# Optimization experiments

Measured on AMD Instinct MI355X. Metric: run time of the kernel, lower is better.

The kernel has to match this reference:

```python
import jax, jax.numpy as jnp
import numpy as np

B, S, D = 1, 2048, 2048
HQ, HKV, DH = 16, 4, 128
WINDOW = 512  # sliding window encoded in explicit attn_mask


def rotate_half(u):
    u1, u2 = jnp.split(u, 2, axis=-1)
    return jnp.concatenate([-u2, u1], axis=-1)


def setup_inputs() -> dict:
    key = jax.random.key(0)
    ks = jax.random.split(key, 6)
    x = jax.random.normal(ks[0], (B, S, D), dtype=jnp.float32)
    # RoPE caches (standard rotary frequencies, full d_head with duplicated halves)
    pos = jnp.arange(S)
    inv_freq = 1.0 / (10000.0 ** (jnp.arange(0, DH, 2, dtype=jnp.float32) / DH))
    ang = pos[:, None].astype(jnp.float32) * inv_freq[None, :]  # [S, DH/2]
    emb = jnp.concatenate([ang, ang], axis=-1)                  # [S, DH]
    cos_cache = jnp.cos(emb)
    sin_cache = jnp.sin(emb)
    # sliding-window causal mask: attend to j<=i and i-j < WINDOW
    i = jnp.arange(S)[:, None]
    j = jnp.arange(S)[None, :]
    attn_mask = (j <= i) & ((i - j) < WINDOW)
    sc = 0.02
    Wq = jax.random.normal(ks[1], (D, HQ * DH), dtype=jnp.float32) * sc
    Wk = jax.random.normal(ks[2], (D, HKV * DH), dtype=jnp.float32) * sc
    Wv = jax.random.normal(ks[3], (D, HKV * DH), dtype=jnp.float32) * sc
    Wo = jax.random.normal(ks[4], (HQ * DH, D), dtype=jnp.float32) * sc
    return {"x": x, "cos_cache": cos_cache, "sin_cache": sin_cache,
            "positions": pos.astype(jnp.int64), "attn_mask": attn_mask,
            "Wq": Wq, "Wk": Wk, "Wv": Wv, "Wo": Wo}


def reference(x, cos_cache, sin_cache, positions, attn_mask, Wq, Wk, Wv, Wo):
    batch, seq_len, _ = x.shape
    Q = (x @ Wq).reshape(batch, seq_len, HQ, DH).transpose(0, 2, 1, 3)   # [B,HQ,S,DH]
    K = (x @ Wk).reshape(batch, seq_len, HKV, DH).transpose(0, 2, 1, 3)  # [B,HKV,S,DH]
    V = (x @ Wv).reshape(batch, seq_len, HKV, DH).transpose(0, 2, 1, 3)
    # RoPE
    cos = cos_cache[positions][None, None, :, :]  # [1,1,S,DH]
    sin = sin_cache[positions][None, None, :, :]
    Q = Q * cos + rotate_half(Q) * sin
    K = K * cos + rotate_half(K) * sin
    # GQA expansion (repeat_interleave along head dim)
    G = HQ // HKV
    K_exp = jnp.repeat(K, G, axis=1)  # [B,HQ,S,DH]
    V_exp = jnp.repeat(V, G, axis=1)
    scores = jnp.einsum('bhqd,bhkd->bhqk', Q, K_exp) / jnp.sqrt(jnp.float32(DH))
    neg_inf = jnp.finfo(scores.dtype).min
    scores = jnp.where(attn_mask[None, None, :, :], scores, neg_inf)
    weights = jax.nn.softmax(scores, axis=-1)
    attn_out = jnp.einsum('bhqk,bhkd->bhqd', weights, V_exp)
    attn_out = attn_out.transpose(0, 2, 1, 3).reshape(batch, seq_len, HQ * DH)
    output = attn_out @ Wo
    return (output, K, V)  # new kv cache is the (post-RoPE) K, V
```

## Files before the change

### kernel.cpp

```cpp
#include <hip/hip_runtime.h>
#include <stdint.h>

typedef unsigned short u16;
typedef __attribute__((ext_vector_type(4))) float f32x4;
typedef __attribute__((ext_vector_type(8))) short short8;
typedef __attribute__((ext_vector_type(4))) short short4v;

__device__ inline u16 f2bf(float f) {
  union { float f; uint32_t u; } v; v.f = f;
  uint32_t u = v.u;
  u += 0x7fffu + ((u >> 16) & 1u);
  return (u16)(u >> 16);
}
__device__ inline float bf2f(u16 b) {
  union { uint32_t u; float f; } v; v.u = (uint32_t)b << 16; return v.f;
}

__global__ __launch_bounds__(256) void k_prep(const float* __restrict__ x,
                                              const float* __restrict__ Wq, const float* __restrict__ Wk,
                                              const float* __restrict__ Wv, const float* __restrict__ Wo,
                                              u16* __restrict__ xb, u16* __restrict__ WT, u16* __restrict__ WoT) {
  const int b = blockIdx.x, tid = threadIdx.x;
  if (b < 1024) {
    size_t base = (size_t)b * 4096 + tid * 4;
    #pragma unroll
    for (int k = 0; k < 4; ++k) {
      f32x4 v = *(const f32x4*)(x + base + k * 1024);
      short4v o;
      o.x = (short)f2bf(v.x); o.y = (short)f2bf(v.y);
      o.z = (short)f2bf(v.z); o.w = (short)f2bf(v.w);
      *(short4v*)(xb + base + k * 1024) = o;
    }
    return;
  }
  __shared__ float t[64][68];
  const float* W; u16* D; int N, bb;
  if (b < 2048)      { W = Wq; D = WT;                       N = 2048; bb = b - 1024; }
  else if (b < 2304) { W = Wk; D = WT + (size_t)2048 * 2048; N = 512;  bb = b - 2048; }
  else if (b < 2560) { W = Wv; D = WT + (size_t)2560 * 2048; N = 512;  bb = b - 2304; }
  else               { W = Wo; D = WoT;                      N = 2048; bb = b - 2560; }
  const int nb = N >> 6;
  const int n0 = (bb % nb) * 64, k0 = (bb / nb) * 64;
  const int c4 = (tid & 15) * 4, rbase = tid >> 4;
  #pragma unroll
  for (int p = 0; p < 4; ++p) {
    int r = p * 16 + rbase;
    *(f32x4*)&t[r][c4] = *(const f32x4*)&W[(size_t)(k0 + r) * N + n0 + c4];
  }
  __syncthreads();
  const int i = tid >> 2, j = (tid & 3) * 16;
  short8 o0, o1;
  #pragma unroll
  for (int m = 0; m < 8; ++m) o0[m] = (short)f2bf(t[j + m][i]);
  #pragma unroll
  for (int m = 0; m < 8; ++m) o1[m] = (short)f2bf(t[j + 8 + m][i]);
  *(short8*)&D[(size_t)(n0 + i) * 2048 + k0 + j] = o0;
  *(short8*)&D[(size_t)(n0 + i) * 2048 + k0 + j + 8] = o1;
}

__global__ __launch_bounds__(512, 2) void k_gemmqkv(const u16* __restrict__ A,
                                                    const u16* __restrict__ B,
                                                    u16* __restrict__ C) {
  const int K = 2048;
  const int NT = 32;
  __shared__ __align__(16) u16 lds[3 * 20480];
  const int tid = threadIdx.x;
  const int wid = tid >> 6, lane = tid & 63;
  const int quad = lane >> 4, l16 = lane & 15;
  const int wm = (wid >> 2) * 64;
  const int wn = (wid & 3) * 48;
  const int bm = blockIdx.y * 128, bn = blockIdx.x * 192;

  const u16* aSrc[2]; int aDst[2];
  #pragma unroll
  for (int L = 0; L < 2; ++L) {
    int E = (tid + L * 512) * 8;
    int r = E >> 6, pc = (E >> 3) & 7;
    int lc = pc ^ (r & 7);
    aSrc[L] = A + (size_t)(bm + r) * K + lc * 8;
    aDst[L] = E;
  }
  const u16* bSrc[3]; int bDst[3];
  #pragma unroll
  for (int L = 0; L < 3; ++L) {
    int E = (tid + L * 512) * 8;
    int r = E >> 6, pc = (E >> 3) & 7;
    int lc = pc ^ (r & 7);
    bSrc[L] = B + (size_t)(bn + r) * K + lc * 8;
    bDst[L] = 8192 + E;
  }

  #define STAGE(buf, kt) do {                                                              \
    _Pragma("unroll")                                                                      \
    for (int L = 0; L < 2; ++L)                                                            \
      __builtin_amdgcn_global_load_lds(                                                    \
          (const __attribute__((address_space(1))) void*)(aSrc[L] + (kt) * 64),            \
          (__attribute__((address_space(3))) void*)(&lds[(buf) * 20480 + aDst[L]]), 16, 0, 0); \
    _Pragma("unroll")                                                                      \
    for (int L = 0; L < 3; ++L)                                                            \
      __builtin_amdgcn_global_load_lds(                                                    \
          (const __attribute__((address_space(1))) void*)(bSrc[L] + (kt) * 64),            \
          (__attribute__((address_space(3))) void*)(&lds[(buf) * 20480 + bDst[L]]), 16, 0, 0); \
  } while (0)

  f32x4 acc[4][3];
  #pragma unroll
  for (int m = 0; m < 4; ++m)
    #pragma unroll
    for (int n = 0; n < 3; ++n) acc[m][n] = (f32x4){0.f, 0.f, 0.f, 0.f};

  STAGE(0, 0);
  STAGE(1, 1);
  asm volatile("s_waitcnt vmcnt(5)" ::: "memory");
  __builtin_amdgcn_s_barrier();

  int c = 0, p = 2;
  for (int t = 0; t < NT; ++t) {
    if (t + 2 < NT) STAGE(p, t + 2);

    short8 af[4][2], bf[3][2];
    #pragma unroll
    for (int mf = 0; mf < 4; ++mf)
      #pragma unroll
      for (int kc = 0; kc < 2; ++kc) {
        int R = wm + mf * 16 + l16;
        int pc = (kc * 4 + quad) ^ (R & 7);
        af[mf][kc] = *(const short8*)&lds[c * 20480 + R * 64 + pc * 8];
      }
    #pragma unroll
    for (int nf = 0; nf < 3; ++nf)
      #pragma unroll
      for (int kc = 0; kc < 2; ++kc) {
        int Cc = wn + nf * 16 + l16;
        int pc = (kc * 4 + quad) ^ (Cc & 7);
        bf[nf][kc] = *(const short8*)&lds[c * 20480 + 8192 + Cc * 64 + pc * 8];
      }

    __builtin_amdgcn_s_setprio(1);
    #pragma unroll
    for (int mf = 0; mf < 4; ++mf)
      #pragma unroll
      for (int nf = 0; nf < 3; ++nf)
        #pragma unroll
        for (int kc = 0; kc < 2; ++kc)
          acc[mf][nf] = __builtin_amdgcn_mfma_f32_16x16x32_bf16(af[mf][kc], bf[nf][kc], acc[mf][nf], 0, 0, 0);
    __builtin_amdgcn_s_setprio(0);

    if (t + 2 < NT) {
      asm volatile("s_waitcnt vmcnt(5)" ::: "memory");
    } else if (t + 1 < NT) {
      asm volatile("s_waitcnt vmcnt(0)" ::: "memory");
    }
    __builtin_amdgcn_s_barrier();
    c = (c == 2) ? 0 : c + 1;
    p = (p == 2) ? 0 : p + 1;
  }
  #undef STAGE

  #pragma unroll
  for (int mf = 0; mf < 4; ++mf) {
    int row = bm + wm + mf * 16 + quad * 4;
    #pragma unroll
    for (int nf = 0; nf < 3; ++nf) {
      int col = bn + wn + nf * 16 + l16;
      #pragma unroll
      for (int r = 0; r < 4; ++r)
        C[(size_t)(row + r) * 3072 + col] = f2bf(acc[mf][nf][r]);
    }
  }
}

__global__ __launch_bounds__(256) void k_gemm64(const u16* __restrict__ A,
                                                const u16* __restrict__ B,
                                                u16* __restrict__ C,
                                                int M, int N, int K) {
  __shared__ u16 As[2][128 * 32];
  __shared__ u16 Bs[2][128 * 32];
  const int tid = threadIdx.x;
  const int wid = tid >> 6, lane = tid & 63;
  const int quad = lane >> 4, l16 = lane & 15;
  const int wm = (wid >> 1) * 64, wn = (wid & 1) * 64;
  const int bm = blockIdx.y * 128, bn = blockIdx.x * 128;
  const int lr = lane >> 2;
  const int lc = (lane & 3) * 8;
  const int kper = K / gridDim.z;
  const int kbeg = blockIdx.z * kper;
  u16* Cz = C + (size_t)blockIdx.z * M * N;

  f32x4 acc[4][4];
  #pragma unroll
  for (int mi = 0; mi < 4; ++mi)
    #pragma unroll
    for (int ni = 0; ni < 4; ++ni)
      acc[mi][ni] = (f32x4){0.f, 0.f, 0.f, 0.f};

  for (int k0 = kbeg; k0 < kbeg + kper; k0 += 64) {
    const u16* Ag = A + (size_t)bm * K + k0;
    const u16* Bg = B + (size_t)bn * K + k0;
    #pragma unroll
    for (int h = 0; h < 2; ++h)
      #pragma unroll
      for (int p = 0; p < 2; ++p) {
        const int r0 = wid * 32 + p * 16;
        const int rr = r0 + lr;
        __builtin_amdgcn_global_load_lds(
            (const __attribute__((address_space(1))) void*)(Ag + (size_t)rr * K + h * 32 + lc),
            (__attribute__((address_space(3))) void*)(&As[h][r0 * 32]),
            16, 0, 0);
        __builtin_amdgcn_global_load_lds(
            (const __attribute__((address_space(1))) void*)(Bg + (size_t)rr * K + h * 32 + lc),
            (__attribute__((address_space(3))) void*)(&Bs[h][r0 * 32]),
            16, 0, 0);
      }
    __syncthreads();
    #pragma unroll
    for (int h = 0; h < 2; ++h) {
      short8 af[4], bfr[4];
      #pragma unroll
      for (int i = 0; i < 4; ++i) {
        af[i]  = *(const short8*)&As[h][(wm + i * 16 + l16) * 32 + quad * 8];
        bfr[i] = *(const short8*)&Bs[h][(wn + i * 16 + l16) * 32 + quad * 8];
      }
      #pragma unroll
      for (int mi = 0; mi < 4; ++mi)
        #pragma unroll
        for (int ni = 0; ni < 4; ++ni)
          acc[mi][ni] = __builtin_amdgcn_mfma_f32_16x16x32_bf16(af[mi], bfr[ni], acc[mi][ni], 0, 0, 0);
    }
    __syncthreads();
  }
  #pragma unroll
  for (int mi = 0; mi < 4; ++mi) {
    int row = bm + wm + mi * 16 + quad * 4;
    #pragma unroll
    for (int ni = 0; ni < 4; ++ni) {
      int col = bn + wn + ni * 16 + l16;
      #pragma unroll
      for (int r = 0; r < 4; ++r)
        Cz[(size_t)(row + r) * N + col] = f2bf(acc[mi][ni][r]);
    }
  }
}

__global__ __launch_bounds__(256) void k_post(const u16* __restrict__ P,
                                              const float* __restrict__ cosc, const float* __restrict__ sinc,
                                              u16* __restrict__ Qb, u16* __restrict__ Kb, u16* __restrict__ Vt,
                                              float* __restrict__ Kout, float* __restrict__ Vout) {
  const int b = blockIdx.x, tid = threadIdx.x;
  if (b < 2048) {
    __shared__ float row[3072];
    const int s = b;
    const u16* p0 = P + (size_t)s * 3072;
    for (int i = tid * 4; i < 3072; i += 1024) {
      short4v a0 = *(const short4v*)(p0 + i);
      #pragma unroll
      for (int m = 0; m < 4; ++m)
        row[i + m] = bf2f((u16)a0[m]);
    }
    __syncthreads();
    const int d = tid & 127;
    const int hbase = tid >> 7;
    const float c = cosc[s * 128 + d], sn = sinc[s * 128 + d];
    const float scale = 0.08838834764831845f;
    #pragma unroll
    for (int it = 0; it < 12; ++it) {
      int slice = it * 2 + hbase;
      float v = row[slice * 128 + d];
      if (slice < 20) {
        float other = (d < 64) ? -row[slice * 128 + d + 64] : row[slice * 128 + d - 64];
        float r = v * c + other * sn;
        if (slice < 16) {
          Qb[((size_t)slice * 2048 + s) * 128 + d] = f2bf(r * scale);
        } else {
          int hk = slice - 16;
          Kout[((size_t)hk * 2048 + s) * 128 + d] = r;
          Kb[((size_t)hk * 2048 + s) * 128 + d] = f2bf(r);
        }
      } else {
        int hv = slice - 20;
        Vout[((size_t)hv * 2048 + s) * 128 + d] = v;
      }
    }
  } else {
    __shared__ float t[32][33];
    const int b2 = b - 2048;
    const int c0 = (b2 & 15) * 32, s0 = (b2 >> 4) * 32;
    const int tx = tid & 31, ty = tid >> 5;
    #pragma unroll
    for (int i = ty; i < 32; i += 8) {
      size_t idx = (size_t)(s0 + i) * 3072 + 2560 + c0 + tx;
      t[i][tx] = bf2f(P[idx]);
    }
    __syncthreads();
    const int head = c0 >> 7, dbase = c0 & 127;
    #pragma unroll
    for (int i = ty; i < 32; i += 8)
      Vt[((size_t)head * 128 + dbase + i) * 2048 + s0 + tx] = f2bf(t[tx][i]);
  }
}

__global__ __launch_bounds__(512) void k_attn(const u16* __restrict__ Qb,
                                              const u16* __restrict__ Kb,
                                              const u16* __restrict__ Vt,
                                              u16* __restrict__ O) {
  const int qt = blockIdx.x;
  const int hk = blockIdx.y;
  const int tid = threadIdx.x;
  const int wid = tid >> 6, lane = tid & 63;
  const int quad = lane >> 4, l16 = lane & 15;
  const int h = hk * 4 + (wid >> 1);
  const int qrow0 = qt * 32;
  const int r0 = qrow0 + (wid & 1) * 16;
  const u16* Qh = Qb + (size_t)h * 2048 * 128;
  const u16* Kh = Kb + (size_t)hk * 2048 * 128;
  const u16* Vh = Vt + (size_t)hk * 128 * 2048;

  __shared__ u16 Ks[32 * 136];
  __shared__ u16 Vs[128 * 40];
  __shared__ u16 Ps[8][16 * 40];

  short8 qa[4];
  #pragma unroll
  for (int ks = 0; ks < 4; ++ks)
    qa[ks] = *(const short8*)&Qh[(size_t)(r0 + l16) * 128 + ks * 32 + quad * 8];

  f32x4 o[8];
  #pragma unroll
  for (int dt = 0; dt < 8; ++dt) o[dt] = (f32x4){0.f, 0.f, 0.f, 0.f};
  float lsum[4] = {0.f, 0.f, 0.f, 0.f};

  const int c0 = qrow0 > 511 ? (qrow0 - 511) >> 5 : 0;
  const int c1 = (qrow0 + 31) >> 5;

  short8 kreg, vreg;
  {
    const int jb = c0 * 32;
    kreg = *(const short8*)&Kh[(size_t)(jb + (tid >> 4)) * 128 + (tid & 15) * 8];
    vreg = *(const short8*)&Vh[(size_t)(tid >> 2) * 2048 + jb + (tid & 3) * 8];
  }

  for (int c = c0; c <= c1; ++c) {
    const int jbase = c * 32;
    __syncthreads();
    *(short8*)&Ks[(tid >> 4) * 136 + (tid & 15) * 8] = kreg;
    *(short8*)&Vs[(tid >> 2) * 40  + (tid & 3)  * 8] = vreg;
    if (c < c1) {
      const int jb = jbase + 32;
      kreg = *(const short8*)&Kh[(size_t)(jb + (tid >> 4)) * 128 + (tid & 15) * 8];
      vreg = *(const short8*)&Vh[(size_t)(tid >> 2) * 2048 + jb + (tid & 3) * 8];
    }
    __syncthreads();

    f32x4 sc[2];
    #pragma unroll
    for (int ni = 0; ni < 2; ++ni) {
      sc[ni] = (f32x4){0.f, 0.f, 0.f, 0.f};
      #pragma unroll
      for (int ks = 0; ks < 4; ++ks) {
        short8 kf = *(const short8*)&Ks[(ni * 16 + l16) * 136 + ks * 32 + quad * 8];
        sc[ni] = __builtin_amdgcn_mfma_f32_16x16x32_bf16(qa[ks], kf, sc[ni], 0, 0, 0);
      }
    }
    #pragma unroll
    for (int ni = 0; ni < 2; ++ni) {
      const int jlo = jbase + ni * 16;
      const bool none = (jlo > r0 + 15) || (jlo + 15 < r0 - 511);
      const bool allv = (jlo + 15 <= r0) && (jlo >= r0 - 496);
      float p[4];
      if (none) {
        p[0] = p[1] = p[2] = p[3] = 0.f;
      } else if (allv) {
        #pragma unroll
        for (int r = 0; r < 4; ++r) p[r] = __expf(sc[ni][r]);
      } else {
        const int j = jlo + l16;
        #pragma unroll
        for (int r = 0; r < 4; ++r) {
          int i = r0 + quad * 4 + r;
          bool ok = (j <= i) && (i - j < 512);
          p[r] = ok ? __expf(sc[ni][r]) : 0.f;
        }
      }
      #pragma unroll
      for (int r = 0; r < 4; ++r) {
        lsum[r] += p[r];
        Ps[wid][(quad * 4 + r) * 40 + ni * 16 + l16] = f2bf(p[r]);
      }
    }
    short8 pa = *(const short8*)&Ps[wid][l16 * 40 + quad * 8];
    #pragma unroll
    for (int dt = 0; dt < 8; ++dt) {
      short8 vf = *(const short8*)&Vs[(dt * 16 + l16) * 40 + quad * 8];
      o[dt] = __builtin_amdgcn_mfma_f32_16x16x32_bf16(pa, vf, o[dt], 0, 0, 0);
    }
  }

  #pragma unroll
  for (int off = 1; off < 16; off <<= 1)
    #pragma unroll
    for (int r = 0; r < 4; ++r)
      lsum[r] += __shfl_xor(lsum[r], off, 64);
  float inv[4];
  #pragma unroll
  for (int r = 0; r < 4; ++r) inv[r] = 1.0f / lsum[r];

  #pragma unroll
  for (int dt = 0; dt < 8; ++dt) {
    int col = h * 128 + dt * 16 + l16;
    #pragma unroll
    for (int r = 0; r < 4; ++r) {
      int row = r0 + quad * 4 + r;
      O[(size_t)row * 2048 + col] = f2bf(o[dt][r] * inv[r]);
    }
  }
}

__global__ __launch_bounds__(256) void k_add2(const u16* __restrict__ P, float* __restrict__ C) {
  const size_t st = (size_t)2048 * 2048;
  size_t i = ((size_t)blockIdx.x * 256 + threadIdx.x) * 8;
  short8 a = *(const short8*)(P + i);
  short8 b = *(const short8*)(P + st + i);
  f32x4 lo, hi;
  #pragma unroll
  for (int m = 0; m < 4; ++m)
    lo[m] = bf2f((u16)a[m]) + bf2f((u16)b[m]);
  #pragma unroll
  for (int m = 0; m < 4; ++m)
    hi[m] = bf2f((u16)a[m + 4]) + bf2f((u16)b[m + 4]);
  *(f32x4*)(C + i) = lo;
  *(f32x4*)(C + i + 4) = hi;
}

extern "C" void kernel_launch(void* const* d_in, const int* in_sizes, int n_in,
                              void* d_out, int out_size, void* d_ws, size_t ws_size,
                              hipStream_t stream) {
  const float* x    = (const float*)d_in[0];
  const float* cosc = (const float*)d_in[1];
  const float* sinc = (const float*)d_in[2];
  const float* Wq = (const float*)d_in[5];
  const float* Wk = (const float*)d_in[6];
  const float* Wv = (const float*)d_in[7];
  const float* Wo = (const float*)d_in[8];

  char* ws = (char*)d_ws;
  u16*   xb    = (u16*)(ws);
  u16*   O     = (u16*)(ws);
  u16*   WT    = (u16*)(ws + (8u  << 20));
  u16*   WoT   = (u16*)(ws + (20u << 20));
  u16*   Qb    = (u16*)(ws + (28u << 20));
  u16*   Kb    = (u16*)(ws + (36u << 20));
  u16*   Vt    = (u16*)(ws + (38u << 20));
  u16*   QKV   = (u16*)(ws + (40u << 20));
  u16*   Op    = (u16*)(ws + (40u << 20));

  float* outO = (float*)d_out;
  float* outK = (float*)d_out + 4194304;
  float* outV = (float*)d_out + 5242880;

  k_prep<<<3584, 256, 0, stream>>>(x, Wq, Wk, Wv, Wo, xb, WT, WoT);
  k_gemmqkv<<<dim3(16, 16), 512, 0, stream>>>(xb, WT, QKV);
  k_post<<<3072, 256, 0, stream>>>(QKV, cosc, sinc, Qb, Kb, Vt, outK, outV);
  k_attn<<<dim3(64, 4), 512, 0, stream>>>(Qb, Kb, Vt, O);
  k_gemm64<<<dim3(16, 16, 2), 256, 0, stream>>>(O, WoT, Op, 2048, 2048, 2048);
  k_add2<<<2048, 256, 0, stream>>>(Op, outO);
}
```

Measured before the change: 112.4 us.

## Replace split-K output GEMM and add kernel with pipelined single-pass GEMM

Replaces the split-K output projection, which wrote two bf16 partials and then ran a separate add kernel, with a single GEMM that covers the full K and writes fp32 directly. The new kernel uses 512 threads, a three-stage LDS ring fed by global_load_lds, an XOR swizzle against bank conflicts, and s_setprio around the MFMAs. This drops one launch and the round trip of the partial buffers through memory, and it also avoids rounding the final output to bf16. The cost is only 256 blocks with no split-K, which may reduce parallelism on the many CUs.

```diff
diff --git a/kernel.cpp b/kernel.cpp
--- a/kernel.cpp
+++ b/kernel.cpp
@@ -170,74 +170,106 @@
   }
 }
 
-__global__ __launch_bounds__(256) void k_gemm64(const u16* __restrict__ A,
-                                                const u16* __restrict__ B,
-                                                u16* __restrict__ C,
-                                                int M, int N, int K) {
-  __shared__ u16 As[2][128 * 32];
-  __shared__ u16 Bs[2][128 * 32];
+__global__ __launch_bounds__(512, 2) void k_gemmo(const u16* __restrict__ A,
+                                                  const u16* __restrict__ B,
+                                                  float* __restrict__ C) {
+  const int K = 2048;
+  const int NT = 32;
+  __shared__ __align__(16) u16 lds[3 * 16384];
   const int tid = threadIdx.x;
   const int wid = tid >> 6, lane = tid & 63;
   const int quad = lane >> 4, l16 = lane & 15;
-  const int wm = (wid >> 1) * 64, wn = (wid & 1) * 64;
+  const int wm = (wid >> 2) * 64;
+  const int wn = (wid & 3) * 32;
   const int bm = blockIdx.y * 128, bn = blockIdx.x * 128;
-  const int lr = lane >> 2;
-  const int lc = (lane & 3) * 8;
-  const int kper = K / gridDim.z;
-  const int kbeg = blockIdx.z * kper;
-  u16* Cz = C + (size_t)blockIdx.z * M * N;
-
-  f32x4 acc[4][4];
-  #pragma unroll
-  for (int mi = 0; mi < 4; ++mi)
-    #pragma unroll
-    for (int ni = 0; ni < 4; ++ni)
-      acc[mi][ni] = (f32x4){0.f, 0.f, 0.f, 0.f};
-
-  for (int k0 = kbeg; k0 < kbeg + kper; k0 += 64) {
-    const u16* Ag = A + (size_t)bm * K + k0;
-    const u16* Bg = B + (size_t)bn * K + k0;
-    #pragma unroll
-    for (int h = 0; h < 2; ++h)
-      #pragma unroll
-      for (int p = 0; p < 2; ++p) {
-        const int r0 = wid * 32 + p * 16;
-        const int rr = r0 + lr;
-        __builtin_amdgcn_global_load_lds(
-            (const __attribute__((address_space(1))) void*)(Ag + (size_t)rr * K + h * 32 + lc),
-            (__attribute__((address_space(3))) void*)(&As[h][r0 * 32]),
-            16, 0, 0);
-        __builtin_amdgcn_global_load_lds(
-            (const __attribute__((address_space(1))) void*)(Bg + (size_t)rr * K + h * 32 + lc),
-            (__attribute__((address_space(3))) void*)(&Bs[h][r0 * 32]),
-            16, 0, 0);
-      }
-    __syncthreads();
-    #pragma unroll
-    for (int h = 0; h < 2; ++h) {
-      short8 af[4], bfr[4];
-      #pragma unroll
-      for (int i = 0; i < 4; ++i) {
-        af[i]  = *(const short8*)&As[h][(wm + i * 16 + l16) * 32 + quad * 8];
-        bfr[i] = *(const short8*)&Bs[h][(wn + i * 16 + l16) * 32 + quad * 8];
-      }
-      #pragma unroll
-      for (int mi = 0; mi < 4; ++mi)
+
+  const u16* aSrc[2]; const u16* bSrc[2]; int dDst[2];
+  #pragma unroll
+  for (int L = 0; L < 2; ++L) {
+    int E = (tid + L * 512) * 8;
+    int r = E >> 6, pc = (E >> 3) & 7;
+    int lc = pc ^ (r & 7);
+    aSrc[L] = A + (size_t)(bm + r) * K + lc * 8;
+    bSrc[L] = B + (size_t)(bn + r) * K + lc * 8;
+    dDst[L] = E;
+  }
+
+  #define STAGEO(buf, kt) do {                                                             \
+    _Pragma("unroll")                                                                      \
+    for (int L = 0; L < 2; ++L)                                                            \
+      __builtin_amdgcn_global_load_lds(                                                    \
+          (const __attribute__((address_space(1))) void*)(aSrc[L] + (kt) * 64),            \
+          (__attribute__((address_space(3))) void*)(&lds[(buf) * 16384 + dDst[L]]), 16, 0, 0); \
+    _Pragma("unroll")                                                                      \
+    for (int L = 0; L < 2; ++L)                                                            \
+      __builtin_amdgcn_global_load_lds(                                                    \
+          (const __attribute__((address_space(1))) void*)(bSrc[L] + (kt) * 64),            \
+          (__attribute__((address_space(3))) void*)(&lds[(buf) * 16384 + 8192 + dDst[L]]), 16, 0, 0); \
+  } while (0)
+
+  f32x4 acc[4][2];
+  #pragma unroll
+  for (int m = 0; m < 4; ++m)
+    #pragma unroll
+    for (int n = 0; n < 2; ++n) acc[m][n] = (f32x4){0.f, 0.f, 0.f, 0.f};
+
+  STAGEO(0, 0);
+  STAGEO(1, 1);
+  asm volatile("s_waitcnt vmcnt(4)" ::: "memory");
+  __builtin_amdgcn_s_barrier();
+
+  int c = 0, p = 2;
+  for (int t = 0; t < NT; ++t) {
+    if (t + 2 < NT) STAGEO(p, t + 2);
+
+    short8 af[4][2], bf[2][2];
+    #pragma unroll
+    for (int mf = 0; mf < 4; ++mf)
+      #pragma unroll
+      for (int kc = 0; kc < 2; ++kc) {
+        int R = wm + mf * 16 + l16;
+        int pc = (kc * 4 + quad) ^ (R & 7);
+        af[mf][kc] = *(const short8*)&lds[c * 16384 + R * 64 + pc * 8];
+      }
+    #pragma unroll
+    for (int nf = 0; nf < 2; ++nf)
+      #pragma unroll
+      for (int kc = 0; kc < 2; ++kc) {
+        int Cc = wn + nf * 16 + l16;
+        int pc = (kc * 4 + quad) ^ (Cc & 7);
+        bf[nf][kc] = *(const short8*)&lds[c * 16384 + 8192 + Cc * 64 + pc * 8];
+      }
+
+    __builtin_amdgcn_s_setprio(1);
+    #pragma unroll
+    for (int mf = 0; mf < 4; ++mf)
+      #pragma unroll
+      for (int nf = 0; nf < 2; ++nf)
         #pragma unroll
-        for (int ni = 0; ni < 4; ++ni)
-          acc[mi][ni] = __builtin_amdgcn_mfma_f32_16x16x32_bf16(af[mi], bfr[ni], acc[mi][ni], 0, 0, 0);
-    }
-    __syncthreads();
-  }
-  #pragma unroll
-  for (int mi = 0; mi < 4; ++mi) {
-    int row = bm + wm + mi * 16 + quad * 4;
-    #pragma unroll
-    for (int ni = 0; ni < 4; ++ni) {
-      int col = bn + wn + ni * 16 + l16;
+        for (int kc = 0; kc < 2; ++kc)
+          acc[mf][nf] = __builtin_amdgcn_mfma_f32_16x16x32_bf16(af[mf][kc], bf[nf][kc], acc[mf][nf], 0, 0, 0);
+    __builtin_amdgcn_s_setprio(0);
+
+    if (t + 2 < NT) {
+      asm volatile("s_waitcnt vmcnt(4)" ::: "memory");
+    } else if (t + 1 < NT) {
+      asm volatile("s_waitcnt vmcnt(0)" ::: "memory");
+    }
+    __builtin_amdgcn_s_barrier();
+    c = (c == 2) ? 0 : c + 1;
+    p = (p == 2) ? 0 : p + 1;
+  }
+  #undef STAGEO
+
+  #pragma unroll
+  for (int mf = 0; mf < 4; ++mf) {
+    int row = bm + wm + mf * 16 + quad * 4;
+    #pragma unroll
+    for (int nf = 0; nf < 2; ++nf) {
+      int col = bn + wn + nf * 16 + l16;
       #pragma unroll
       for (int r = 0; r < 4; ++r)
-        Cz[(size_t)(row + r) * N + col] = f2bf(acc[mi][ni][r]);
+        C[(size_t)(row + r) * 2048 + col] = acc[mf][nf][r];
     }
   }
 }
@@ -415,22 +447,6 @@
   }
 }
 
-__global__ __launch_bounds__(256) void k_add2(const u16* __restrict__ P, float* __restrict__ C) {
-  const size_t st = (size_t)2048 * 2048;
-  size_t i = ((size_t)blockIdx.x * 256 + threadIdx.x) * 8;
-  short8 a = *(const short8*)(P + i);
-  short8 b = *(const short8*)(P + st + i);
-  f32x4 lo, hi;
-  #pragma unroll
-  for (int m = 0; m < 4; ++m)
-    lo[m] = bf2f((u16)a[m]) + bf2f((u16)b[m]);
-  #pragma unroll
-  for (int m = 0; m < 4; ++m)
-    hi[m] = bf2f((u16)a[m + 4]) + bf2f((u16)b[m + 4]);
-  *(f32x4*)(C + i) = lo;
-  *(f32x4*)(C + i + 4) = hi;
-}
-
 extern "C" void kernel_launch(void* const* d_in, const int* in_sizes, int n_in,
                               void* d_out, int out_size, void* d_ws, size_t ws_size,
                               hipStream_t stream) {
@@ -451,7 +467,6 @@
   u16*   Kb    = (u16*)(ws + (36u << 20));
   u16*   Vt    = (u16*)(ws + (38u << 20));
   u16*   QKV   = (u16*)(ws + (40u << 20));
-  u16*   Op    = (u16*)(ws + (40u << 20));
 
   float* outO = (float*)d_out;
   float* outK = (float*)d_out + 4194304;
@@ -461,6 +476,5 @@
   k_gemmqkv<<<dim3(16, 16), 512, 0, stream>>>(xb, WT, QKV);
   k_post<<<3072, 256, 0, stream>>>(QKV, cosc, sinc, Qb, Kb, Vt, outK, outV);
   k_attn<<<dim3(64, 4), 512, 0, stream>>>(Qb, Kb, Vt, O);
-  k_gemm64<<<dim3(16, 16, 2), 256, 0, stream>>>(O, WoT, Op, 2048, 2048, 2048);
-  k_add2<<<2048, 256, 0, stream>>>(Op, outO);
-}
+  k_gemmo<<<dim3(16, 16), 512, 0, stream>>>(O, WoT, outO);
+}
```

Measured after the change: 102.4 us. 8.8% less time.
